# Kernel tuning notes

Hardware: AMD Instinct MI355X
Metric: run time of the kernel (lower is better)

Reference implementation:

```python
import jax, jax.numpy as jnp
import numpy as np

# ---- architecture constants (from init_kwargs / arch_args) ----
B, CIN, H, W = 2, 128, 32, 32
COUT, K, PAD = 128, 3, 1
IB, FRAC, NSTREAMS = 8, 8, 8     # input bits, input frac bits, 1-bit streams
WB, NSLICES = 8, 8               # weight bits, 1-bit slices
ADC_BITS = 4
NSUB = 9                         # ceil(128*9 / subarray_size=128); 1152/9 = 128 (even chunks)


def ste_round(x):
    # straight-through round
    return x + jax.lax.stop_gradient(jnp.round(x) - x)


def unfold(x, k, pad):
    # torch F.unfold (im2col), channel-major (c, kh, kw) feature ordering
    xp = jnp.pad(x, ((0, 0), (0, 0), (pad, pad), (pad, pad)))
    Ho = x.shape[2] + 2 * pad - k + 1
    Wo = x.shape[3] + 2 * pad - k + 1
    cols = [xp[:, :, i:i + Ho, j:j + Wo] for i in range(k) for j in range(k)]
    p = jnp.stack(cols, axis=2)              # [B, C, k*k, Ho, Wo]
    return p.reshape(x.shape[0], -1, Ho * Wo), Ho, Wo


def bit_streams(patches):
    # quantize unsigned fixed-point then decompose into 1-bit streams (STE)
    xi = jnp.clip(ste_round(patches * (2.0 ** FRAC)), 0.0, 2.0 ** IB - 1.0)  # [B,F,P]
    shifts = 2.0 ** jnp.arange(NSTREAMS, dtype=jnp.float32)
    bits = jnp.floor(jax.lax.stop_gradient(xi)[..., None] / shifts) % 2.0
    share = xi[..., None] / (NSTREAMS * shifts)  # equal-split STE grad path (recombines to identity)
    return share + jax.lax.stop_gradient(bits - share)  # [B,F,P,S]


def bit_slices(w):
    # per-out-channel normalization, signed int quantization, pos/neg 1-bit slices (STE)
    norm = jax.lax.stop_gradient(jnp.max(jnp.abs(w.reshape(w.shape[0], -1)), axis=1))  # [O]
    Q = 2.0 ** WB - 1.0
    wi = ste_round(w / norm[:, None, None, None] * Q)  # in [-Q, Q]
    shifts = 2.0 ** jnp.arange(NSLICES, dtype=jnp.float32)

    def slices(m):
        b = jnp.floor(jax.lax.stop_gradient(m)[..., None] / shifts) % 2.0
        share = m[..., None] / (NSLICES * shifts)
        return share + jax.lax.stop_gradient(b - share)

    pos = slices(jax.nn.relu(wi)).reshape(w.shape[0], -1, NSLICES)   # [O, F, T]
    neg = slices(jax.nn.relu(-wi)).reshape(w.shape[0], -1, NSLICES)  # [O, F, T]
    return pos, neg, norm


def adc(ps):
    # N-bit ADC quantization of non-negative partial sums, dynamic full-scale, STE
    levels = 2.0 ** ADC_BITS - 1.0
    vmax = jnp.maximum(jax.lax.stop_gradient(jnp.max(ps)), 1e-6)
    step = vmax / levels
    return jnp.clip(ste_round(ps / step), 0.0, levels) * step


def _forward(inputs, weight):
    patches, Ho, Wo = unfold(inputs, K, PAD)          # [B, CIN*K*K, P]
    streams = bit_streams(patches)                     # [B, F, P, S]
    pos_w, neg_w, norm = bit_slices(weight)            # [O, F, T]
    ss = (2.0 ** jnp.arange(NSTREAMS, dtype=jnp.float32)).reshape(1, 1, 1, -1, 1)
    ts = (2.0 ** jnp.arange(NSLICES, dtype=jnp.float32)).reshape(1, 1, 1, 1, -1)

    s_chunks = jnp.split(streams, NSUB, axis=1)
    p_chunks = jnp.split(pos_w, NSUB, axis=1)
    n_chunks = jnp.split(neg_w, NSUB, axis=1)

    out = jnp.zeros((inputs.shape[0], COUT, Ho * Wo), jnp.float32)
    for sc, pc, nc in zip(s_chunks, p_chunks, n_chunks):  # fixed NSUB=9 subarrays
        pr = jnp.einsum('bfps,oft->bopst', sc, pc)  # [B,O,P,S,T] per-subarray MVM
        nr = jnp.einsum('bfps,oft->bopst', sc, nc)
        out = out + ((adc(pr) - adc(nr)) * ss * ts).sum(axis=(-2, -1))

    Q = 2.0 ** WB - 1.0
    out = out * norm[None, :, None] / Q / (2.0 ** IB)
    return out.reshape(inputs.shape[0], COUT, Ho, Wo)


def setup_inputs() -> dict:
    key = jax.random.key(0)
    k1, k2 = jax.random.split(key)
    inputs = jax.random.uniform(k1, (B, CIN, H, W), dtype=jnp.float32)
    fan_in = CIN * K * K
    weight = jax.random.normal(k2, (COUT, CIN, K, K), dtype=jnp.float32) * np.float32(np.sqrt(2.0 / fan_in))
    return {"inputs": inputs, "weight": weight}


def reference(inputs, weight):
    output = _forward(inputs, weight)
    adc_loss = jnp.float32(0.0)  # adc_custom_loss=False
    return output, adc_loss
```

## Files before the change

kernel.cpp:

```cpp
#include <hip/hip_runtime.h>
#include <stdint.h>

#define B_    2
#define CIN   128
#define HIMG  32
#define WIMG  32
#define COUT_ 128
#define PP    1024
#define FTOT  1152
#define NSUB  9
#define NS    8
#define NT    8
#define NROW  18

typedef int v4i __attribute__((ext_vector_type(4)));

#define OFF_NORM   0
#define OFF_MAXV   512
#define OFF_MB     640
#define OFF_PMODE  800
#define OFF_LUT    1024
#define OFF_WQP    4096
#define OFF_WQN    (4096 + 147456)
#define OFF_XQ     (4096 + 2*147456)

__global__ __launch_bounds__(256) void k_prep_w(const float* __restrict__ w,
                                                float* __restrict__ norm_out,
                                                uint8_t* __restrict__ wqp,
                                                uint8_t* __restrict__ wqn) {
    int o = blockIdx.x, tid = threadIdx.x;
    __shared__ float red[256];
    const float* wo = w + (size_t)o * FTOT;
    float m = 0.f;
    for (int f = tid; f < FTOT; f += 256) m = fmaxf(m, fabsf(wo[f]));
    red[tid] = m;
    __syncthreads();
    for (int s2 = 128; s2 > 0; s2 >>= 1) {
        if (tid < s2) red[tid] = fmaxf(red[tid], red[tid + s2]);
        __syncthreads();
    }
    float norm = red[0];
    if (tid == 0) norm_out[o] = norm;
    for (int f = tid; f < FTOT; f += 256) {
        double wi = rint(((double)wo[f] / (double)norm) * 255.0);
        wqp[(size_t)o * FTOT + f] = (uint8_t)(int)fmax(wi, 0.0);
        wqn[(size_t)o * FTOT + f] = (uint8_t)(int)fmax(-wi, 0.0);
    }
}

__global__ __launch_bounds__(256) void k_prep_x(const float* __restrict__ x,
                                                uint8_t* __restrict__ xq,
                                                uint32_t* __restrict__ maxv) {
    if (blockIdx.x == 0 && threadIdx.x < NROW) maxv[threadIdx.x] = 0u;
    int gid = blockIdx.x * 256 + threadIdx.x;
    int fg = gid % 72;
    int rest = gid / 72;
    int p = rest & 1023;
    int b = rest >> 10;
    int py = p >> 5, px = p & 31;
    uint32_t dw[4] = {0, 0, 0, 0};
    #pragma unroll
    for (int j = 0; j < 16; ++j) {
        int f = fg * 16 + j;
        int c = f / 9, u = f % 9;
        int kh = u / 3, kw = u % 3;
        int y = py + kh - 1, xx = px + kw - 1;
        uint32_t xi = 0;
        if (y >= 0 && y < HIMG && xx >= 0 && xx < WIMG) {
            float v = x[(((size_t)b * CIN + c) * HIMG + y) * WIMG + xx];
            float q = rintf(v * 256.0f);
            q = fminf(fmaxf(q, 0.f), 255.f);
            xi = (uint32_t)q;
        }
        dw[j >> 2] |= xi << ((j & 3) * 8);
    }
    *reinterpret_cast<uint4*>(xq + (size_t)((b << 10) + p) * FTOT + fg * 16) =
        make_uint4(dw[0], dw[1], dw[2], dw[3]);
}

__device__ __forceinline__ v4i bitsel(uint4 d, int sh) {
    v4i r;
    r[0] = (int)((d.x >> sh) & 0x01010101u);
    r[1] = (int)((d.y >> sh) & 0x01010101u);
    r[2] = (int)((d.z >> sh) & 0x01010101u);
    r[3] = (int)((d.w >> sh) & 0x01010101u);
    return r;
}

__global__ __launch_bounds__(512) void k_max(const uint8_t* __restrict__ xq,
                                             const uint8_t* __restrict__ wqp,
                                             const uint8_t* __restrict__ wqn,
                                             uint32_t* __restrict__ maxv) {
    int tid = threadIdx.x, lane = tid & 63, wid = tid >> 6;
    int blk = blockIdx.x;
    int b = blk >> 9, r = blk & 511, ot = r >> 6, pt = r & 63;
    int t = wid;
    int col = lane & 15, kq = lane >> 4;
    int p = pt * 16 + col, oa = ot * 16 + col;
    __shared__ uint32_t smax[8][NSUB][2];

    const uint8_t* xbase = xq + (size_t)((b << 10) + p) * FTOT + kq * 16;
    const uint8_t* wpb = wqp + (size_t)oa * FTOT + kq * 16;
    const uint8_t* wnb = wqn + (size_t)oa * FTOT + kq * 16;

    for (int sub = 0; sub < NSUB; ++sub) {
        int fo = sub * 128;
        uint4 wp0 = *(const uint4*)(wpb + fo), wp1 = *(const uint4*)(wpb + fo + 64);
        uint4 wn0 = *(const uint4*)(wnb + fo), wn1 = *(const uint4*)(wnb + fo + 64);
        v4i ap0 = bitsel(wp0, t), ap1 = bitsel(wp1, t);
        v4i an0 = bitsel(wn0, t), an1 = bitsel(wn1, t);
        uint4 xg0 = *(const uint4*)(xbase + fo);
        uint4 xg1 = *(const uint4*)(xbase + fo + 64);

        int mp = 0, mn = 0;
        #pragma unroll
        for (int s = 0; s < NS; ++s) {
            v4i bf0 = bitsel(xg0, s), bf1 = bitsel(xg1, s);
            v4i acc = {0, 0, 0, 0};
            acc = __builtin_amdgcn_mfma_i32_16x16x64_i8(ap0, bf0, acc, 0, 0, 0);
            acc = __builtin_amdgcn_mfma_i32_16x16x64_i8(ap1, bf1, acc, 0, 0, 0);
            mp = max(mp, max(max(acc[0], acc[1]), max(acc[2], acc[3])));
            v4i acn = {0, 0, 0, 0};
            acn = __builtin_amdgcn_mfma_i32_16x16x64_i8(an0, bf0, acn, 0, 0, 0);
            acn = __builtin_amdgcn_mfma_i32_16x16x64_i8(an1, bf1, acn, 0, 0, 0);
            mn = max(mn, max(max(acn[0], acn[1]), max(acn[2], acn[3])));
        }
        #pragma unroll
        for (int off = 32; off > 0; off >>= 1) {
            mp = max(mp, __shfl_xor(mp, off));
            mn = max(mn, __shfl_xor(mn, off));
        }
        if (lane == 0) { smax[wid][sub][0] = (uint32_t)mp; smax[wid][sub][1] = (uint32_t)mn; }
    }
    __syncthreads();
    if (tid < NROW) {
        int sub = tid >> 1, sg = tid & 1;
        uint32_t m = 0;
        #pragma unroll
        for (int w2 = 0; w2 < 8; ++w2) m = max(m, smax[w2][sub][sg]);
        atomicMax(&maxv[tid], m);
    }
}

__global__ __launch_bounds__(256) void k_lut(const uint32_t* __restrict__ maxv,
                                             uint8_t* __restrict__ lut,
                                             uint2* __restrict__ mb,
                                             int* __restrict__ pmode) {
    int row = blockIdx.x, tid = threadIdx.x;
    __shared__ uint8_t codes[132];
    __shared__ int bestm;
    if (tid == 0) bestm = 0x7fffffff;
    int vmax = (int)maxv[row];
    for (int pr = tid; pr < 129; pr += 256) {
        double vmaxd = fmax((double)vmax, 1e-6);
        double step = vmaxd / 15.0;
        double q = rint((double)pr / step);
        q = fmin(fmax(q, 0.0), 15.0);
        codes[pr] = (uint8_t)q;
        lut[row * 132 + pr] = (uint8_t)q;
    }
    __syncthreads();
    int ve = max(vmax, 1);
    int m0 = (983040 + ve / 2) / ve;
    int m = m0 - 128 + tid;
    if (m >= 1) {
        int L = 0, U = 0x7fffffff;
        for (int pr = 0; pr <= vmax && pr <= 128; ++pr) {
            int c = codes[pr];
            int lo = (c << 16) - pr * m;
            int hi = ((c + 1) << 16) - 1 - pr * m;
            L = max(L, lo);
            U = min(U, hi);
            if (L > U) break;
        }
        if (L <= U) atomicMin(&bestm, m);
    }
    __syncthreads();
    if (tid == 0) {
        if (bestm == 0x7fffffff) {
            pmode[row] = 1;
            mb[row] = make_uint2(0u, 0u);
        } else {
            int L = 0;
            for (int pr = 0; pr <= vmax && pr <= 128; ++pr)
                L = max(L, ((int)codes[pr] << 16) - pr * bestm);
            pmode[row] = 0;
            mb[row] = make_uint2((uint32_t)bestm, (uint32_t)L);
        }
    }
}

__global__ __launch_bounds__(512) void k_adc(const uint8_t* __restrict__ xq,
                                             const uint8_t* __restrict__ wqp,
                                             const uint8_t* __restrict__ wqn,
                                             const uint32_t* __restrict__ maxv,
                                             const uint8_t* __restrict__ lut,
                                             const uint2* __restrict__ mb,
                                             const int* __restrict__ pmode,
                                             const float* __restrict__ norm,
                                             float* __restrict__ out) {
    int tid = threadIdx.x, lane = tid & 63, wid = tid >> 6;
    int blk = blockIdx.x;
    int b = blk >> 9, r = blk & 511, ot = r >> 6, pt = r & 63;
    int t = wid;
    int col = lane & 15, kq = lane >> 4;
    int p = pt * 16 + col, oa = ot * 16 + col;

    __shared__ int lred[8][64][4];

    const uint8_t* xbase = xq + (size_t)((b << 10) + p) * FTOT + kq * 16;
    const uint8_t* wpb = wqp + (size_t)oa * FTOT + kq * 16;
    const uint8_t* wnb = wqn + (size_t)oa * FTOT + kq * 16;

    int run[4] = {0, 0, 0, 0};
    for (int sub = 0; sub < NSUB; ++sub) {
        int fo = sub * 128;
        uint4 wp0 = *(const uint4*)(wpb + fo), wp1 = *(const uint4*)(wpb + fo + 64);
        uint4 wn0 = *(const uint4*)(wnb + fo), wn1 = *(const uint4*)(wnb + fo + 64);
        v4i ap0 = bitsel(wp0, t), ap1 = bitsel(wp1, t);
        v4i an0 = bitsel(wn0, t), an1 = bitsel(wn1, t);
        uint4 xg0 = *(const uint4*)(xbase + fo);
        uint4 xg1 = *(const uint4*)(xbase + fo + 64);

        int rowp = sub * 2, rown = sub * 2 + 1;
        uint2 mbp = mb[rowp], mbn = mb[rown];
        int fbp = pmode[rowp], fbn = pmode[rown];
        const uint8_t* glp = lut + rowp * 132;
        const uint8_t* gln = lut + rown * 132;
        int vp = (int)maxv[rowp], vn = (int)maxv[rown];

        uint32_t Sp[4] = {0, 0, 0, 0}, Sn[4] = {0, 0, 0, 0};
        #pragma unroll
        for (int s = 0; s < NS; ++s) {
            v4i bf0 = bitsel(xg0, s), bf1 = bitsel(xg1, s);
            v4i acc = {0, 0, 0, 0};
            acc = __builtin_amdgcn_mfma_i32_16x16x64_i8(ap0, bf0, acc, 0, 0, 0);
            acc = __builtin_amdgcn_mfma_i32_16x16x64_i8(ap1, bf1, acc, 0, 0, 0);
            if (fbp == 0) {
                #pragma unroll
                for (int i = 0; i < 4; ++i) {
                    uint32_t v = __umul24((uint32_t)acc[i], mbp.x) + mbp.y;
                    Sp[i] += ((v >> 16) & 15u) << s;
                }
            } else {
                #pragma unroll
                for (int i = 0; i < 4; ++i) Sp[i] += (uint32_t)glp[acc[i]] << s;
            }
            v4i acn = {0, 0, 0, 0};
            acn = __builtin_amdgcn_mfma_i32_16x16x64_i8(an0, bf0, acn, 0, 0, 0);
            acn = __builtin_amdgcn_mfma_i32_16x16x64_i8(an1, bf1, acn, 0, 0, 0);
            if (fbn == 0) {
                #pragma unroll
                for (int i = 0; i < 4; ++i) {
                    uint32_t v = __umul24((uint32_t)acn[i], mbn.x) + mbn.y;
                    Sn[i] += ((v >> 16) & 15u) << s;
                }
            } else {
                #pragma unroll
                for (int i = 0; i < 4; ++i) Sn[i] += (uint32_t)gln[acn[i]] << s;
            }
        }
        #pragma unroll
        for (int i = 0; i < 4; ++i) {
            int d = (int)__umul24((uint32_t)vp, Sp[i]) - (int)__umul24((uint32_t)vn, Sn[i]);
            run[i] += (int)((uint32_t)d << t);
        }
    }
    #pragma unroll
    for (int i = 0; i < 4; ++i) lred[wid][lane][i] = run[i];
    __syncthreads();
    if (tid < 256) {
        int lane2 = tid >> 2, i = tid & 3;
        long long s64 = 0;
        #pragma unroll
        for (int w2 = 0; w2 < 8; ++w2) s64 += (long long)lred[w2][lane2][i];
        int o = ot * 16 + (lane2 >> 4) * 4 + i;
        int pp2 = pt * 16 + (lane2 & 15);
        double v = (double)s64 * (double)norm[o] / 15.0 / 255.0 / 256.0;
        out[((size_t)(b * COUT_ + o)) * PP + pp2] = (float)v;
    }
    if (blk == 0 && tid == 0) out[(size_t)B_ * COUT_ * PP] = 0.0f;
}

extern "C" void kernel_launch(void* const* d_in, const int* in_sizes, int n_in,
                              void* d_out, int out_size, void* d_ws, size_t ws_size,
                              hipStream_t stream) {
    const float* x = (const float*)d_in[0];
    const float* w = (const float*)d_in[1];
    float* out = (float*)d_out;
    char* ws = (char*)d_ws;

    float* norm = (float*)(ws + OFF_NORM);
    uint32_t* maxv = (uint32_t*)(ws + OFF_MAXV);
    uint2* mb = (uint2*)(ws + OFF_MB);
    int* pmode = (int*)(ws + OFF_PMODE);
    uint8_t* lut = (uint8_t*)(ws + OFF_LUT);
    uint8_t* wqp = (uint8_t*)(ws + OFF_WQP);
    uint8_t* wqn = (uint8_t*)(ws + OFF_WQN);
    uint8_t* xq  = (uint8_t*)(ws + OFF_XQ);

    k_prep_w<<<128, 256, 0, stream>>>(w, norm, wqp, wqn);
    k_prep_x<<<576, 256, 0, stream>>>(x, xq, maxv);
    k_max<<<1024, 512, 0, stream>>>(xq, wqp, wqn, maxv);
    k_lut<<<NROW, 256, 0, stream>>>(maxv, lut, mb, pmode);
    k_adc<<<1024, 512, 0, stream>>>(xq, wqp, wqn, maxv, lut, mb, pmode, norm, out);
}
```

Before: 170.4 us.

## Stage bit-sliced weights in swizzled LDS and swap wave mapping to input streams

Each wave now owns one input bit-stream instead of one weight slice. All eight weight slices (pos and neg) are expanded once per subarray by the whole block into a swizzled shared-memory buffer, and every wave reads them from there. This removes the redundant per-wave global weight loads and bitsel work, and hoists the input bitsel out of the inner loop. The cost is two block barriers per subarray and 32KB of LDS per block, which may lower occupancy. The shift accounting is adjusted so the combined shift (s+t) is applied per partial sum.

```diff
diff --git a/kernel.cpp b/kernel.cpp
--- a/kernel.cpp
+++ b/kernel.cpp
@@ -23,6 +23,8 @@
 #define OFF_WQP    4096
 #define OFF_WQN    (4096 + 147456)
 #define OFF_XQ     (4096 + 2*147456)
+
+#define SWZ16(o, koff) ((koff) ^ (((o) & 7) << 4))
 
 __global__ __launch_bounds__(256) void k_prep_w(const float* __restrict__ w,
                                                 float* __restrict__ norm_out,
@@ -94,28 +96,44 @@
     int tid = threadIdx.x, lane = tid & 63, wid = tid >> 6;
     int blk = blockIdx.x;
     int b = blk >> 9, r = blk & 511, ot = r >> 6, pt = r & 63;
-    int t = wid;
+    int s = wid;
     int col = lane & 15, kq = lane >> 4;
-    int p = pt * 16 + col, oa = ot * 16 + col;
+    int p = pt * 16 + col;
+
+    __shared__ uint8_t wlds[32768];
     __shared__ uint32_t smax[8][NSUB][2];
 
     const uint8_t* xbase = xq + (size_t)((b << 10) + p) * FTOT + kq * 16;
-    const uint8_t* wpb = wqp + (size_t)oa * FTOT + kq * 16;
-    const uint8_t* wnb = wqn + (size_t)oa * FTOT + kq * 16;
+    int a0 = col * 128 + SWZ16(col, kq * 16);
+    int a1 = a0 ^ 64;
+
+    int it = tid >> 1, th = tid & 1;
+    int skq = it & 7, so = (it >> 3) & 15, ssign = it >> 7;
+    const uint8_t* ssrc = (ssign ? wqn : wqp) + (size_t)(ot * 16 + so) * FTOT + skq * 16;
+    int swb = so * 128 + SWZ16(so, skq * 16);
 
     for (int sub = 0; sub < NSUB; ++sub) {
-        int fo = sub * 128;
-        uint4 wp0 = *(const uint4*)(wpb + fo), wp1 = *(const uint4*)(wpb + fo + 64);
-        uint4 wn0 = *(const uint4*)(wnb + fo), wn1 = *(const uint4*)(wnb + fo + 64);
-        v4i ap0 = bitsel(wp0, t), ap1 = bitsel(wp1, t);
-        v4i an0 = bitsel(wn0, t), an1 = bitsel(wn1, t);
-        uint4 xg0 = *(const uint4*)(xbase + fo);
-        uint4 xg1 = *(const uint4*)(xbase + fo + 64);
+        {
+            uint4 d = *(const uint4*)(ssrc + sub * 128);
+            #pragma unroll
+            for (int j = 0; j < 4; ++j) {
+                int t = th * 4 + j;
+                *(v4i*)&wlds[(t * 2 + ssign) * 2048 + swb] = bitsel(d, t);
+            }
+        }
+        __syncthreads();
+
+        uint4 xg0 = *(const uint4*)(xbase + sub * 128);
+        uint4 xg1 = *(const uint4*)(xbase + sub * 128 + 64);
+        v4i bf0 = bitsel(xg0, s), bf1 = bitsel(xg1, s);
 
         int mp = 0, mn = 0;
         #pragma unroll
-        for (int s = 0; s < NS; ++s) {
-            v4i bf0 = bitsel(xg0, s), bf1 = bitsel(xg1, s);
+        for (int t = 0; t < NT; ++t) {
+            v4i ap0 = *(const v4i*)&wlds[(t * 2 + 0) * 2048 + a0];
+            v4i ap1 = *(const v4i*)&wlds[(t * 2 + 0) * 2048 + a1];
+            v4i an0 = *(const v4i*)&wlds[(t * 2 + 1) * 2048 + a0];
+            v4i an1 = *(const v4i*)&wlds[(t * 2 + 1) * 2048 + a1];
             v4i acc = {0, 0, 0, 0};
             acc = __builtin_amdgcn_mfma_i32_16x16x64_i8(ap0, bf0, acc, 0, 0, 0);
             acc = __builtin_amdgcn_mfma_i32_16x16x64_i8(ap1, bf1, acc, 0, 0, 0);
@@ -131,8 +149,8 @@
             mn = max(mn, __shfl_xor(mn, off));
         }
         if (lane == 0) { smax[wid][sub][0] = (uint32_t)mp; smax[wid][sub][1] = (uint32_t)mn; }
-    }
-    __syncthreads();
+        __syncthreads();
+    }
     if (tid < NROW) {
         int sub = tid >> 1, sg = tid & 1;
         uint32_t m = 0;
@@ -202,25 +220,37 @@
     int tid = threadIdx.x, lane = tid & 63, wid = tid >> 6;
     int blk = blockIdx.x;
     int b = blk >> 9, r = blk & 511, ot = r >> 6, pt = r & 63;
-    int t = wid;
+    int s = wid;
     int col = lane & 15, kq = lane >> 4;
-    int p = pt * 16 + col, oa = ot * 16 + col;
-
-    __shared__ int lred[8][64][4];
+    int p = pt * 16 + col;
+
+    __shared__ uint8_t wlds[32768];
+    int (*lred)[64][4] = (int (*)[64][4])wlds;
 
     const uint8_t* xbase = xq + (size_t)((b << 10) + p) * FTOT + kq * 16;
-    const uint8_t* wpb = wqp + (size_t)oa * FTOT + kq * 16;
-    const uint8_t* wnb = wqn + (size_t)oa * FTOT + kq * 16;
+    int a0 = col * 128 + SWZ16(col, kq * 16);
+    int a1 = a0 ^ 64;
+
+    int it = tid >> 1, th = tid & 1;
+    int skq = it & 7, so = (it >> 3) & 15, ssign = it >> 7;
+    const uint8_t* ssrc = (ssign ? wqn : wqp) + (size_t)(ot * 16 + so) * FTOT + skq * 16;
+    int swb = so * 128 + SWZ16(so, skq * 16);
 
     int run[4] = {0, 0, 0, 0};
     for (int sub = 0; sub < NSUB; ++sub) {
-        int fo = sub * 128;
-        uint4 wp0 = *(const uint4*)(wpb + fo), wp1 = *(const uint4*)(wpb + fo + 64);
-        uint4 wn0 = *(const uint4*)(wnb + fo), wn1 = *(const uint4*)(wnb + fo + 64);
-        v4i ap0 = bitsel(wp0, t), ap1 = bitsel(wp1, t);
-        v4i an0 = bitsel(wn0, t), an1 = bitsel(wn1, t);
-        uint4 xg0 = *(const uint4*)(xbase + fo);
-        uint4 xg1 = *(const uint4*)(xbase + fo + 64);
+        {
+            uint4 d = *(const uint4*)(ssrc + sub * 128);
+            #pragma unroll
+            for (int j = 0; j < 4; ++j) {
+                int t = th * 4 + j;
+                *(v4i*)&wlds[(t * 2 + ssign) * 2048 + swb] = bitsel(d, t);
+            }
+        }
+        __syncthreads();
+
+        uint4 xg0 = *(const uint4*)(xbase + sub * 128);
+        uint4 xg1 = *(const uint4*)(xbase + sub * 128 + 64);
+        v4i bf0 = bitsel(xg0, s), bf1 = bitsel(xg1, s);
 
         int rowp = sub * 2, rown = sub * 2 + 1;
         uint2 mbp = mb[rowp], mbn = mb[rown];
@@ -231,20 +261,23 @@
 
         uint32_t Sp[4] = {0, 0, 0, 0}, Sn[4] = {0, 0, 0, 0};
         #pragma unroll
-        for (int s = 0; s < NS; ++s) {
-            v4i bf0 = bitsel(xg0, s), bf1 = bitsel(xg1, s);
+        for (int t = 0; t < NT; ++t) {
+            v4i ap0 = *(const v4i*)&wlds[(t * 2 + 0) * 2048 + a0];
+            v4i ap1 = *(const v4i*)&wlds[(t * 2 + 0) * 2048 + a1];
+            v4i an0 = *(const v4i*)&wlds[(t * 2 + 1) * 2048 + a0];
+            v4i an1 = *(const v4i*)&wlds[(t * 2 + 1) * 2048 + a1];
             v4i acc = {0, 0, 0, 0};
             acc = __builtin_amdgcn_mfma_i32_16x16x64_i8(ap0, bf0, acc, 0, 0, 0);
             acc = __builtin_amdgcn_mfma_i32_16x16x64_i8(ap1, bf1, acc, 0, 0, 0);
             if (fbp == 0) {
                 #pragma unroll
                 for (int i = 0; i < 4; ++i) {
-                    uint32_t v = __umul24((uint32_t)acc[i], mbp.x) + mbp.y;
-                    Sp[i] += ((v >> 16) & 15u) << s;
+                    uint32_t q = ((__umul24((uint32_t)acc[i], mbp.x) + mbp.y) >> 16) & 15u;
+                    Sp[i] += q << (s + t);
                 }
             } else {
                 #pragma unroll
-                for (int i = 0; i < 4; ++i) Sp[i] += (uint32_t)glp[acc[i]] << s;
+                for (int i = 0; i < 4; ++i) Sp[i] += (uint32_t)glp[acc[i]] << (s + t);
             }
             v4i acn = {0, 0, 0, 0};
             acn = __builtin_amdgcn_mfma_i32_16x16x64_i8(an0, bf0, acn, 0, 0, 0);
@@ -252,20 +285,20 @@
             if (fbn == 0) {
                 #pragma unroll
                 for (int i = 0; i < 4; ++i) {
-                    uint32_t v = __umul24((uint32_t)acn[i], mbn.x) + mbn.y;
-                    Sn[i] += ((v >> 16) & 15u) << s;
+                    uint32_t q = ((__umul24((uint32_t)acn[i], mbn.x) + mbn.y) >> 16) & 15u;
+                    Sn[i] += q << (s + t);
                 }
             } else {
                 #pragma unroll
-                for (int i = 0; i < 4; ++i) Sn[i] += (uint32_t)gln[acn[i]] << s;
+                for (int i = 0; i < 4; ++i) Sn[i] += (uint32_t)gln[acn[i]] << (s + t);
             }
         }
         #pragma unroll
-        for (int i = 0; i < 4; ++i) {
-            int d = (int)__umul24((uint32_t)vp, Sp[i]) - (int)__umul24((uint32_t)vn, Sn[i]);
-            run[i] += (int)((uint32_t)d << t);
-        }
-    }
+        for (int i = 0; i < 4; ++i)
+            run[i] += (int)__umul24((uint32_t)vp, Sp[i]) - (int)__umul24((uint32_t)vn, Sn[i]);
+        __syncthreads();
+    }
+
     #pragma unroll
     for (int i = 0; i < 4; ++i) lred[wid][lane][i] = run[i];
     __syncthreads();
```

After: 150.5 us. -11.7%, faster.

## Precompute weight bit-slices into an MFMA-ready layout and split waves over slices and streams

Applied to the files above, without the earlier changes.

The weight prep kernel now writes bit-sliced weights (per subarray, slice and sign) directly in the operand layout the MFMA expects. This removes the per-wave weight bit extraction in k_max and k_adc. Each wave now covers 2 weight slices × 4 input streams instead of 1 slice × all 8 streams, with the slice shift folded into the per-product shift. A launch_bounds occupancy hint is added. In exchange, each wave loads more weight data per subarray, and the prep kernel gains an extra shared-memory pass.

```diff
diff --git a/kernel.cpp b/kernel.cpp
--- a/kernel.cpp
+++ b/kernel.cpp
@@ -20,16 +20,25 @@
 #define OFF_MB     640
 #define OFF_PMODE  800
 #define OFF_LUT    1024
-#define OFF_WQP    4096
-#define OFF_WQN    (4096 + 147456)
-#define OFF_XQ     (4096 + 2*147456)
+#define OFF_XQ     4096
+#define OFF_WBY    2363392
+
+__device__ __forceinline__ v4i bitsel(uint4 d, int sh) {
+    v4i r;
+    r[0] = (int)((d.x >> sh) & 0x01010101u);
+    r[1] = (int)((d.y >> sh) & 0x01010101u);
+    r[2] = (int)((d.z >> sh) & 0x01010101u);
+    r[3] = (int)((d.w >> sh) & 0x01010101u);
+    return r;
+}
 
 __global__ __launch_bounds__(256) void k_prep_w(const float* __restrict__ w,
                                                 float* __restrict__ norm_out,
-                                                uint8_t* __restrict__ wqp,
-                                                uint8_t* __restrict__ wqn) {
+                                                uint8_t* __restrict__ wby) {
     int o = blockIdx.x, tid = threadIdx.x;
     __shared__ float red[256];
+    __shared__ alignas(16) uint8_t sip[FTOT];
+    __shared__ alignas(16) uint8_t sin_[FTOT];
     const float* wo = w + (size_t)o * FTOT;
     float m = 0.f;
     for (int f = tid; f < FTOT; f += 256) m = fmaxf(m, fabsf(wo[f]));
@@ -43,8 +52,17 @@
     if (tid == 0) norm_out[o] = norm;
     for (int f = tid; f < FTOT; f += 256) {
         double wi = rint(((double)wo[f] / (double)norm) * 255.0);
-        wqp[(size_t)o * FTOT + f] = (uint8_t)(int)fmax(wi, 0.0);
-        wqn[(size_t)o * FTOT + f] = (uint8_t)(int)fmax(-wi, 0.0);
+        sip[f] = (uint8_t)(int)fmax(wi, 0.0);
+        sin_[f] = (uint8_t)(int)fmax(-wi, 0.0);
+    }
+    __syncthreads();
+    for (int e = tid; e < 1152; e += 256) {
+        int q4 = e & 7, ts = (e >> 3) & 15, sub = e >> 7;
+        int sign = ts & 1, t = ts >> 1;
+        const uint8_t* src = (sign ? sin_ : sip) + sub * 128 + q4 * 16;
+        uint4 d = *(const uint4*)src;
+        *(v4i*)(wby + (size_t)(((sub * 8 + t) * 2 + sign) * 16384)
+                    + o * 128 + q4 * 16) = bitsel(d, t);
     }
 }
 
@@ -78,52 +96,47 @@
         make_uint4(dw[0], dw[1], dw[2], dw[3]);
 }
 
-__device__ __forceinline__ v4i bitsel(uint4 d, int sh) {
-    v4i r;
-    r[0] = (int)((d.x >> sh) & 0x01010101u);
-    r[1] = (int)((d.y >> sh) & 0x01010101u);
-    r[2] = (int)((d.z >> sh) & 0x01010101u);
-    r[3] = (int)((d.w >> sh) & 0x01010101u);
-    return r;
-}
-
-__global__ __launch_bounds__(512) void k_max(const uint8_t* __restrict__ xq,
-                                             const uint8_t* __restrict__ wqp,
-                                             const uint8_t* __restrict__ wqn,
-                                             uint32_t* __restrict__ maxv) {
+__global__ __launch_bounds__(512, 4) void k_max(const uint8_t* __restrict__ xq,
+                                                const uint8_t* __restrict__ wby,
+                                                uint32_t* __restrict__ maxv) {
     int tid = threadIdx.x, lane = tid & 63, wid = tid >> 6;
     int blk = blockIdx.x;
     int b = blk >> 9, r = blk & 511, ot = r >> 6, pt = r & 63;
-    int t = wid;
+    int tp = wid & 3, sh = wid >> 2;
     int col = lane & 15, kq = lane >> 4;
     int p = pt * 16 + col, oa = ot * 16 + col;
     __shared__ uint32_t smax[8][NSUB][2];
 
     const uint8_t* xbase = xq + (size_t)((b << 10) + p) * FTOT + kq * 16;
-    const uint8_t* wpb = wqp + (size_t)oa * FTOT + kq * 16;
-    const uint8_t* wnb = wqn + (size_t)oa * FTOT + kq * 16;
+    const uint8_t* wbase = wby + (size_t)(tp * 2 * 2) * 16384 + oa * 128 + kq * 16;
 
     for (int sub = 0; sub < NSUB; ++sub) {
-        int fo = sub * 128;
-        uint4 wp0 = *(const uint4*)(wpb + fo), wp1 = *(const uint4*)(wpb + fo + 64);
-        uint4 wn0 = *(const uint4*)(wnb + fo), wn1 = *(const uint4*)(wnb + fo + 64);
-        v4i ap0 = bitsel(wp0, t), ap1 = bitsel(wp1, t);
-        v4i an0 = bitsel(wn0, t), an1 = bitsel(wn1, t);
-        uint4 xg0 = *(const uint4*)(xbase + fo);
-        uint4 xg1 = *(const uint4*)(xbase + fo + 64);
+        const uint8_t* wb = wbase + (size_t)sub * 262144;
+        v4i wf[8];
+        #pragma unroll
+        for (int j = 0; j < 4; ++j) {
+            wf[j * 2]     = *(const v4i*)(wb + j * 16384);
+            wf[j * 2 + 1] = *(const v4i*)(wb + j * 16384 + 64);
+        }
+        uint4 xg0 = *(const uint4*)(xbase + sub * 128);
+        uint4 xg1 = *(const uint4*)(xbase + sub * 128 + 64);
 
         int mp = 0, mn = 0;
         #pragma unroll
-        for (int s = 0; s < NS; ++s) {
+        for (int si = 0; si < 4; ++si) {
+            int s = sh * 4 + si;
             v4i bf0 = bitsel(xg0, s), bf1 = bitsel(xg1, s);
-            v4i acc = {0, 0, 0, 0};
-            acc = __builtin_amdgcn_mfma_i32_16x16x64_i8(ap0, bf0, acc, 0, 0, 0);
-            acc = __builtin_amdgcn_mfma_i32_16x16x64_i8(ap1, bf1, acc, 0, 0, 0);
-            mp = max(mp, max(max(acc[0], acc[1]), max(acc[2], acc[3])));
-            v4i acn = {0, 0, 0, 0};
-            acn = __builtin_amdgcn_mfma_i32_16x16x64_i8(an0, bf0, acn, 0, 0, 0);
-            acn = __builtin_amdgcn_mfma_i32_16x16x64_i8(an1, bf1, acn, 0, 0, 0);
-            mn = max(mn, max(max(acn[0], acn[1]), max(acn[2], acn[3])));
+            #pragma unroll
+            for (int tt = 0; tt < 2; ++tt) {
+                v4i acc = {0, 0, 0, 0};
+                acc = __builtin_amdgcn_mfma_i32_16x16x64_i8(wf[tt * 4 + 0], bf0, acc, 0, 0, 0);
+                acc = __builtin_amdgcn_mfma_i32_16x16x64_i8(wf[tt * 4 + 1], bf1, acc, 0, 0, 0);
+                mp = max(mp, max(max(acc[0], acc[1]), max(acc[2], acc[3])));
+                v4i acn = {0, 0, 0, 0};
+                acn = __builtin_amdgcn_mfma_i32_16x16x64_i8(wf[tt * 4 + 2], bf0, acn, 0, 0, 0);
+                acn = __builtin_amdgcn_mfma_i32_16x16x64_i8(wf[tt * 4 + 3], bf1, acn, 0, 0, 0);
+                mn = max(mn, max(max(acn[0], acn[1]), max(acn[2], acn[3])));
+            }
         }
         #pragma unroll
         for (int off = 32; off > 0; off >>= 1) {
@@ -190,37 +203,37 @@
     }
 }
 
-__global__ __launch_bounds__(512) void k_adc(const uint8_t* __restrict__ xq,
-                                             const uint8_t* __restrict__ wqp,
-                                             const uint8_t* __restrict__ wqn,
-                                             const uint32_t* __restrict__ maxv,
-                                             const uint8_t* __restrict__ lut,
-                                             const uint2* __restrict__ mb,
-                                             const int* __restrict__ pmode,
-                                             const float* __restrict__ norm,
-                                             float* __restrict__ out) {
+__global__ __launch_bounds__(512, 4) void k_adc(const uint8_t* __restrict__ xq,
+                                                const uint8_t* __restrict__ wby,
+                                                const uint32_t* __restrict__ maxv,
+                                                const uint8_t* __restrict__ lut,
+                                                const uint2* __restrict__ mb,
+                                                const int* __restrict__ pmode,
+                                                const float* __restrict__ norm,
+                                                float* __restrict__ out) {
     int tid = threadIdx.x, lane = tid & 63, wid = tid >> 6;
     int blk = blockIdx.x;
     int b = blk >> 9, r = blk & 511, ot = r >> 6, pt = r & 63;
-    int t = wid;
+    int tp = wid & 3, sh = wid >> 2;
     int col = lane & 15, kq = lane >> 4;
     int p = pt * 16 + col, oa = ot * 16 + col;
 
     __shared__ int lred[8][64][4];
 
     const uint8_t* xbase = xq + (size_t)((b << 10) + p) * FTOT + kq * 16;
-    const uint8_t* wpb = wqp + (size_t)oa * FTOT + kq * 16;
-    const uint8_t* wnb = wqn + (size_t)oa * FTOT + kq * 16;
+    const uint8_t* wbase = wby + (size_t)(tp * 2 * 2) * 16384 + oa * 128 + kq * 16;
 
     int run[4] = {0, 0, 0, 0};
     for (int sub = 0; sub < NSUB; ++sub) {
-        int fo = sub * 128;
-        uint4 wp0 = *(const uint4*)(wpb + fo), wp1 = *(const uint4*)(wpb + fo + 64);
-        uint4 wn0 = *(const uint4*)(wnb + fo), wn1 = *(const uint4*)(wnb + fo + 64);
-        v4i ap0 = bitsel(wp0, t), ap1 = bitsel(wp1, t);
-        v4i an0 = bitsel(wn0, t), an1 = bitsel(wn1, t);
-        uint4 xg0 = *(const uint4*)(xbase + fo);
-        uint4 xg1 = *(const uint4*)(xbase + fo + 64);
+        const uint8_t* wb = wbase + (size_t)sub * 262144;
+        v4i wf[8];
+        #pragma unroll
+        for (int j = 0; j < 4; ++j) {
+            wf[j * 2]     = *(const v4i*)(wb + j * 16384);
+            wf[j * 2 + 1] = *(const v4i*)(wb + j * 16384 + 64);
+        }
+        uint4 xg0 = *(const uint4*)(xbase + sub * 128);
+        uint4 xg1 = *(const uint4*)(xbase + sub * 128 + 64);
 
         int rowp = sub * 2, rown = sub * 2 + 1;
         uint2 mbp = mb[rowp], mbn = mb[rown];
@@ -231,40 +244,43 @@
 
         uint32_t Sp[4] = {0, 0, 0, 0}, Sn[4] = {0, 0, 0, 0};
         #pragma unroll
-        for (int s = 0; s < NS; ++s) {
+        for (int si = 0; si < 4; ++si) {
+            int s = sh * 4 + si;
             v4i bf0 = bitsel(xg0, s), bf1 = bitsel(xg1, s);
-            v4i acc = {0, 0, 0, 0};
-            acc = __builtin_amdgcn_mfma_i32_16x16x64_i8(ap0, bf0, acc, 0, 0, 0);
-            acc = __builtin_amdgcn_mfma_i32_16x16x64_i8(ap1, bf1, acc, 0, 0, 0);
-            if (fbp == 0) {
-                #pragma unroll
-                for (int i = 0; i < 4; ++i) {
-                    uint32_t v = __umul24((uint32_t)acc[i], mbp.x) + mbp.y;
-                    Sp[i] += ((v >> 16) & 15u) << s;
+            #pragma unroll
+            for (int tt = 0; tt < 2; ++tt) {
+                int st = s + tp * 2 + tt;
+                v4i acc = {0, 0, 0, 0};
+                acc = __builtin_amdgcn_mfma_i32_16x16x64_i8(wf[tt * 4 + 0], bf0, acc, 0, 0, 0);
+                acc = __builtin_amdgcn_mfma_i32_16x16x64_i8(wf[tt * 4 + 1], bf1, acc, 0, 0, 0);
+                if (fbp == 0) {
+                    #pragma unroll
+                    for (int i = 0; i < 4; ++i) {
+                        uint32_t q = ((__umul24((uint32_t)acc[i], mbp.x) + mbp.y) >> 16) & 15u;
+                        Sp[i] += q << st;
+                    }
+                } else {
+                    #pragma unroll
+                    for (int i = 0; i < 4; ++i) Sp[i] += (uint32_t)glp[acc[i]] << st;
                 }
-            } else {
-                #pragma unroll
-                for (int i = 0; i < 4; ++i) Sp[i] += (uint32_t)glp[acc[i]] << s;
+                v4i acn = {0, 0, 0, 0};
+                acn = __builtin_amdgcn_mfma_i32_16x16x64_i8(wf[tt * 4 + 2], bf0, acn, 0, 0, 0);
+                acn = __builtin_amdgcn_mfma_i32_16x16x64_i8(wf[tt * 4 + 3], bf1, acn, 0, 0, 0);
+                if (fbn == 0) {
+                    #pragma unroll
+                    for (int i = 0; i < 4; ++i) {
+                        uint32_t q = ((__umul24((uint32_t)acn[i], mbn.x) + mbn.y) >> 16) & 15u;
+                        Sn[i] += q << st;
+                    }
+                } else {
+                    #pragma unroll
+                    for (int i = 0; i < 4; ++i) Sn[i] += (uint32_t)gln[acn[i]] << st;
+                }
             }
-            v4i acn = {0, 0, 0, 0};
-            acn = __builtin_amdgcn_mfma_i32_16x16x64_i8(an0, bf0, acn, 0, 0, 0);
-            acn = __builtin_amdgcn_mfma_i32_16x16x64_i8(an1, bf1, acn, 0, 0, 0);
-            if (fbn == 0) {
-                #pragma unroll
-                for (int i = 0; i < 4; ++i) {
-                    uint32_t v = __umul24((uint32_t)acn[i], mbn.x) + mbn.y;
-                    Sn[i] += ((v >> 16) & 15u) << s;
-                }
-            } else {
-                #pragma unroll
-                for (int i = 0; i < 4; ++i) Sn[i] += (uint32_t)gln[acn[i]] << s;
-            }
-        }
-        #pragma unroll
-        for (int i = 0; i < 4; ++i) {
-            int d = (int)__umul24((uint32_t)vp, Sp[i]) - (int)__umul24((uint32_t)vn, Sn[i]);
-            run[i] += (int)((uint32_t)d << t);
-        }
+        }
+        #pragma unroll
+        for (int i = 0; i < 4; ++i)
+            run[i] += vp * (int)Sp[i] - vn * (int)Sn[i];
     }
     #pragma unroll
     for (int i = 0; i < 4; ++i) lred[wid][lane][i] = run[i];
@@ -295,13 +311,12 @@
     uint2* mb = (uint2*)(ws + OFF_MB);
     int* pmode = (int*)(ws + OFF_PMODE);
     uint8_t* lut = (uint8_t*)(ws + OFF_LUT);
-    uint8_t* wqp = (uint8_t*)(ws + OFF_WQP);
-    uint8_t* wqn = (uint8_t*)(ws + OFF_WQN);
     uint8_t* xq  = (uint8_t*)(ws + OFF_XQ);
-
-    k_prep_w<<<128, 256, 0, stream>>>(w, norm, wqp, wqn);
+    uint8_t* wby = (uint8_t*)(ws + OFF_WBY);
+
+    k_prep_w<<<128, 256, 0, stream>>>(w, norm, wby);
     k_prep_x<<<576, 256, 0, stream>>>(x, xq, maxv);
-    k_max<<<1024, 512, 0, stream>>>(xq, wqp, wqn, maxv);
+    k_max<<<1024, 512, 0, stream>>>(xq, wby, maxv);
     k_lut<<<NROW, 256, 0, stream>>>(maxv, lut, mb, pmode);
-    k_adc<<<1024, 512, 0, stream>>>(xq, wqp, wqn, maxv, lut, mb, pmode, norm, out);
-}
+    k_adc<<<1024, 512, 0, stream>>>(xq, wby, maxv, lut, mb, pmode, norm, out);
+}
```

Result: slower. 229.2 us (+34.5%).
